# Performance work log

Measured on AMD Instinct MI355X. Metric: run time of the kernel, lower is better.

## Reference

```python
import jax, jax.numpy as jnp
import numpy as np

TEMPERATURE = 0.8
NEG_FILL = -1e-09  # faithful to original masked_fill value


def setup_inputs() -> dict:
    key = jax.random.key(0)
    k1, k2, k3, k4 = jax.random.split(key, 4)
    B, H, S, D = 2, 16, 2048, 128
    return {
        "key": jax.random.normal(k1, (B, H, S, D), dtype=jnp.float32),
        "value": jax.random.normal(k2, (B, H, S, D), dtype=jnp.float32),
        "query": jax.random.normal(k3, (B, H, S, D), dtype=jnp.float32),
        "mask": jax.random.randint(k4, (1, 1, S, S), 0, 2, dtype=jnp.int32),
    }


def reference(key, value, query, mask) -> jnp.ndarray:
    # scores: [B,H,S,S]
    scores = jnp.einsum("bhqd,bhkd->bhqk", query, key) / TEMPERATURE
    scores = jnp.where(mask == 0, jnp.asarray(NEG_FILL, scores.dtype), scores)
    probs = jax.nn.softmax(scores, axis=-1)
    # dropout p=0.0 -> identity
    return jnp.einsum("bhqk,bhkd->bhqd", probs, value)
```

## Files before the change

kernel.cpp:

```cpp
#include <hip/hip_runtime.h>
#include <hip/hip_bf16.h>
#include <stdint.h>

#define S_LEN 2048
#define HD 128
#define QBLK 128
#define KVBLK 64
#define TPB 512
#define NBH 32
#define NKT (S_LEN / KVBLK)
#define KIMG_TILE 16384

typedef __attribute__((ext_vector_type(8))) _Float16 f16x8;
typedef __attribute__((ext_vector_type(8))) short s16x8;
typedef __attribute__((ext_vector_type(4))) float f32x4;

__device__ __forceinline__ short f2h(float f) {
  _Float16 h = (_Float16)f;
  return __builtin_bit_cast(short, h);
}
__device__ __forceinline__ unsigned short f2b(float f) {
  union { float fv; unsigned u; } v; v.fv = f;
  unsigned r = v.u + 0x7fffu + ((v.u >> 16) & 1u);
  return (unsigned short)(r >> 16);
}
__device__ __forceinline__ float b2f(unsigned short h) {
  union { unsigned u; float fv; } v; v.u = ((unsigned)h) << 16; return v.fv;
}

typedef __attribute__((address_space(3))) uint32_t lds_u32_t;
typedef __attribute__((address_space(1))) const uint32_t glb_u32_t;
__device__ __forceinline__ void gll16(const void* g, void* l) {
  __builtin_amdgcn_global_load_lds((glb_u32_t*)g, (lds_u32_t*)l, 16, 0, 0);
}

__global__ __launch_bounds__(256) void prep_kv(
    const float* __restrict__ Kg, const float* __restrict__ Vg,
    char* __restrict__ KfI, char* __restrict__ VtI) {
  __shared__ __align__(16) char vlds[64 * 528];
  const int t = threadIdx.x;
  const int bh = blockIdx.x >> 5;
  const int kt = blockIdx.x & 31;
  const size_t base = ((size_t)bh * S_LEN + (size_t)kt * KVBLK) * HD;
  const size_t tbase = ((size_t)bh * NKT + kt) * KIMG_TILE;

  {
    const int row = t >> 2;
    const int c4 = (t & 3) * 32;
    const float* src = Kg + base + (size_t)row * HD + c4;
#pragma unroll
    for (int j8 = 0; j8 < 4; ++j8) {
      float4 a = *(const float4*)(src + j8 * 8);
      float4 b = *(const float4*)(src + j8 * 8 + 4);
      float vs[8] = {a.x, a.y, a.z, a.w, b.x, b.y, b.z, b.w};
      s16x8 h;
#pragma unroll
      for (int j = 0; j < 8; ++j) h[j] = f2h(vs[j]);
      int off = (row * 256 + (c4 + j8 * 8) * 2) ^ ((row & 7) << 4);
      *(s16x8*)(KfI + tbase + off) = h;
    }
  }

#pragma unroll
  for (int it = 0; it < 8; ++it) {
    int idx = it * 256 + t;
    int row = idx >> 5;
    int cb = (idx & 31) * 16;
    float4 v = *(const float4*)((const char*)(Vg + base + (size_t)row * HD) + cb);
    *(float4*)(vlds + row * 528 + cb) = v;
  }
  __syncthreads();
  {
    const int d = t & 127;
    const int kvb = (t >> 7) * 32;
#pragma unroll
    for (int jj = 0; jj < 4; ++jj) {
      s16x8 o;
#pragma unroll
      for (int j = 0; j < 8; ++j) {
        int kv = kvb + jj * 8 + j;
        float f = *(const float*)(vlds + kv * 528 + d * 4);
        o[j] = f2h(f);
      }
      int off = (d * 128 + (kvb + jj * 8) * 2) ^ ((d & 7) << 4);
      *(s16x8*)(VtI + tbase + off) = o;
    }
  }
}

#define BUFB 32768
#define SMEMF4 (2 * BUFB + 8 * 2048)

__global__ __launch_bounds__(TPB, 2) void attn_fwd4(
    const char* __restrict__ KfI, const char* __restrict__ VtI,
    const float* __restrict__ Qg, const int* __restrict__ Mg,
    float* __restrict__ Og) {
  __shared__ __align__(16) char smem[SMEMF4];
  char* Psm = smem + 2 * BUFB;

  const int tid = threadIdx.x;
  const int wave = tid >> 6;
  const int lane = tid & 63;
  const int lm = lane & 15;
  const int lg = lane >> 4;

  const int bh = blockIdx.x;
  const int q0 = blockIdx.y * QBLK;
  const int qrow0 = q0 + wave * 16;
  const size_t base = (size_t)bh * S_LEN * HD;
  const float* Qb = Qg + base;

  f16x8 qf[4];
#pragma unroll
  for (int c = 0; c < 4; ++c) {
    const float* src = Qb + (size_t)(qrow0 + lm) * HD + c * 32 + lg * 8;
    float4 a = *(const float4*)src;
    float4 b = *(const float4*)(src + 4);
    float qs[8] = {a.x, a.y, a.z, a.w, b.x, b.y, b.z, b.w};
    f16x8 f;
#pragma unroll
    for (int j = 0; j < 8; ++j) f[j] = (_Float16)(qs[j] * 1.25f);
    qf[c] = f;
  }

  f32x4 acc[8];
#pragma unroll
  for (int i = 0; i < 8; ++i) acc[i] = (f32x4){0.f, 0.f, 0.f, 0.f};
  float mrun[4] = {-1e30f, -1e30f, -1e30f, -1e30f};
  float lrun[4] = {0.f, 0.f, 0.f, 0.f};

  char* Pw = Psm + wave * 2048;
  const int wo = wave * 2048 + lane * 16;

  {
    const size_t tb = (size_t)bh * NKT * KIMG_TILE;
    char* B = smem;
    gll16(KfI + tb + wo,         B + wave * 2048);
    gll16(KfI + tb + wo + 1024,  B + wave * 2048 + 1024);
    gll16(VtI + tb + wo,         B + 16384 + wave * 2048);
    gll16(VtI + tb + wo + 1024,  B + 16384 + wave * 2048 + 1024);
  }
  int mk[4][4], mkn[4][4];
#pragma unroll
  for (int r = 0; r < 4; ++r) {
    const int* mr = Mg + (size_t)(qrow0 + lg * 4 + r) * S_LEN + lm;
#pragma unroll
    for (int st = 0; st < 4; ++st) mk[r][st] = mr[st * 16];
  }

  for (int kt = 0; kt < NKT; ++kt) {
    const int cur = kt & 1;
    char* Bc = smem + cur * BUFB;

    if (kt + 1 < NKT) {
      const size_t tb = ((size_t)bh * NKT + (kt + 1)) * KIMG_TILE;
      char* Bn = smem + (cur ^ 1) * BUFB;
      gll16(KfI + tb + wo,         Bn + wave * 2048);
      gll16(KfI + tb + wo + 1024,  Bn + wave * 2048 + 1024);
      gll16(VtI + tb + wo,         Bn + 16384 + wave * 2048);
      gll16(VtI + tb + wo + 1024,  Bn + 16384 + wave * 2048 + 1024);
      const int kv1 = (kt + 1) * KVBLK;
#pragma unroll
      for (int r = 0; r < 4; ++r) {
        const int* mr = Mg + (size_t)(qrow0 + lg * 4 + r) * S_LEN + kv1 + lm;
#pragma unroll
        for (int st = 0; st < 4; ++st) mkn[r][st] = mr[st * 16];
      }
      asm volatile("s_waitcnt vmcnt(20)" ::: "memory");
    } else {
      asm volatile("s_waitcnt vmcnt(0)" ::: "memory");
    }
    __builtin_amdgcn_sched_barrier(0);
    __builtin_amdgcn_s_barrier();

    __builtin_amdgcn_s_setprio(1);
    f32x4 sf[4];
#pragma unroll
    for (int st = 0; st < 4; ++st) {
      f32x4 c = (f32x4){0.f, 0.f, 0.f, 0.f};
#pragma unroll
      for (int ch = 0; ch < 4; ++ch) {
        int krow = st * 16 + lm;
        int byo = (krow * 256 + ch * 64 + lg * 16) ^ ((krow & 7) << 4);
        f16x8 kf = *(const f16x8*)(Bc + byo);
        c = __builtin_amdgcn_mfma_f32_16x16x32_f16(qf[ch], kf, c, 0, 0, 0);
      }
      sf[st] = c;
    }
    __builtin_amdgcn_s_setprio(0);

    float sc[4][4];
    float mx4[4];
#pragma unroll
    for (int r = 0; r < 4; ++r) {
      float mx = -1e30f;
#pragma unroll
      for (int st = 0; st < 4; ++st) {
        float s = sf[st][r];
        s = mk[r][st] ? s : -1e-9f;
        sc[r][st] = s;
        mx = fmaxf(mx, s);
      }
      mx = fmaxf(mx, __shfl_xor(mx, 1));
      mx = fmaxf(mx, __shfl_xor(mx, 2));
      mx = fmaxf(mx, __shfl_xor(mx, 4));
      mx = fmaxf(mx, __shfl_xor(mx, 8));
      mx4[r] = mx;
    }
    bool need = false;
#pragma unroll
    for (int r = 0; r < 4; ++r) need = need || (mx4[r] > mrun[r] + 8.f);
    if (__any(need)) {
#pragma unroll
      for (int r = 0; r < 4; ++r) {
        float mnew = fmaxf(mrun[r], mx4[r]);
        float scale = __expf(mrun[r] - mnew);
        lrun[r] *= scale;
        mrun[r] = mnew;
#pragma unroll
        for (int dt = 0; dt < 8; ++dt) acc[dt][r] *= scale;
      }
    }
    float pv[4][4];
#pragma unroll
    for (int r = 0; r < 4; ++r) {
      float ps = 0.f;
#pragma unroll
      for (int st = 0; st < 4; ++st) {
        float p = __expf(sc[r][st] - mrun[r]);
        pv[st][r] = p;
        ps += p;
      }
      ps += __shfl_xor(ps, 1);
      ps += __shfl_xor(ps, 2);
      ps += __shfl_xor(ps, 4);
      ps += __shfl_xor(ps, 8);
      lrun[r] += ps;
    }

#pragma unroll
    for (int st = 0; st < 4; ++st) {
#pragma unroll
      for (int r = 0; r < 4; ++r) {
        int row = lg * 4 + r;
        int byo = (row * 128 + (st * 16 + lm) * 2) ^ ((row & 7) << 4);
        *(short*)(Pw + byo) = f2h(pv[st][r]);
      }
    }
    asm volatile("s_waitcnt lgkmcnt(0)" ::: "memory");
    __builtin_amdgcn_sched_barrier(0);

    __builtin_amdgcn_s_setprio(1);
#pragma unroll
    for (int kk = 0; kk < 2; ++kk) {
      f16x8 pa = *(const f16x8*)(Pw + ((lm * 128 + kk * 64 + lg * 16) ^ ((lm & 7) << 4)));
#pragma unroll
      for (int dt = 0; dt < 8; ++dt) {
        int vrow = dt * 16 + lm;
        f16x8 vb = *(const f16x8*)(Bc + 16384 + ((vrow * 128 + kk * 64 + lg * 16) ^ ((lm & 7) << 4)));
        acc[dt] = __builtin_amdgcn_mfma_f32_16x16x32_f16(pa, vb, acc[dt], 0, 0, 0);
      }
    }
    __builtin_amdgcn_s_setprio(0);

    __builtin_amdgcn_sched_barrier(0);
    __builtin_amdgcn_s_barrier();

    if (kt + 1 < NKT) {
#pragma unroll
      for (int r = 0; r < 4; ++r)
#pragma unroll
        for (int st = 0; st < 4; ++st) mk[r][st] = mkn[r][st];
    }
  }

  float invl[4];
#pragma unroll
  for (int r = 0; r < 4; ++r) invl[r] = 1.f / lrun[r];
  float* ob = Og + base;
#pragma unroll
  for (int dt = 0; dt < 8; ++dt) {
#pragma unroll
    for (int r = 0; r < 4; ++r) {
      ob[(size_t)(qrow0 + lg * 4 + r) * HD + dt * 16 + lm] = acc[dt][r] * invl[r];
    }
  }
}

typedef __attribute__((ext_vector_type(8))) short bf16x8;
#define KSM_BYTES (KVBLK * HD * 2)
#define VSM_BYTES (HD * 72 * 2)
#define PSM_PER_WAVE (16 * 72 * 2)
#define SMEM_BYTES (2 * KSM_BYTES + VSM_BYTES + 8 * PSM_PER_WAVE)

__global__ __launch_bounds__(TPB, 2) void attn_fwd(
    const float* __restrict__ Kg, const float* __restrict__ Vg,
    const float* __restrict__ Qg, const int* __restrict__ Mg,
    float* __restrict__ Og) {
  __shared__ __align__(16) char smem[SMEM_BYTES];
  char* KsmH = smem;
  char* KsmL = smem + KSM_BYTES;
  char* Vsm = smem + 2 * KSM_BYTES;
  char* Psm = smem + 2 * KSM_BYTES + VSM_BYTES;

  const int tid = threadIdx.x;
  const int wave = tid >> 6;
  const int lane = tid & 63;
  const int lm = lane & 15;
  const int lg = lane >> 4;

  const int bh = blockIdx.x;
  const int q0 = blockIdx.y * QBLK;
  const int qrow0 = q0 + wave * 16;

  const size_t base = (size_t)bh * S_LEN * HD;
  const float* Kb = Kg + base;
  const float* Vb = Vg + base;
  const float* Qb = Qg + base;

  bf16x8 qhi[4], qlo[4];
#pragma unroll
  for (int c = 0; c < 4; ++c) {
    const float* src = Qb + (size_t)(qrow0 + lm) * HD + c * 32 + lg * 8;
    float4 a = *(const float4*)src;
    float4 b = *(const float4*)(src + 4);
    float qs[8] = {a.x, a.y, a.z, a.w, b.x, b.y, b.z, b.w};
    bf16x8 fh, fl;
#pragma unroll
    for (int j = 0; j < 8; ++j) {
      float v = qs[j] * 1.25f;
      unsigned short h = f2b(v);
      fh[j] = (short)h;
      fl[j] = (short)f2b(v - b2f(h));
    }
    qhi[c] = fh;
    qlo[c] = fl;
  }

  f32x4 acc[8];
#pragma unroll
  for (int i = 0; i < 8; ++i) acc[i] = (f32x4){0.f, 0.f, 0.f, 0.f};
  float mrun[4] = {-1e30f, -1e30f, -1e30f, -1e30f};
  float lrun[4] = {0.f, 0.f, 0.f, 0.f};

  char* Pw = Psm + wave * PSM_PER_WAVE;

  for (int kt = 0; kt < S_LEN / KVBLK; ++kt) {
    const int kv0 = kt * KVBLK;
    int mk[4][4];
#pragma unroll
    for (int r = 0; r < 4; ++r) {
      const int* mr = Mg + (size_t)(qrow0 + lg * 4 + r) * S_LEN + kv0 + lm;
#pragma unroll
      for (int st = 0; st < 4; ++st) mk[r][st] = mr[st * 16];
    }
    __syncthreads();
#pragma unroll
    for (int it = 0; it < 4; ++it) {
      int row = it * 16 + (tid >> 5);
      int col = (tid & 31) * 4;
      float4 v = *(const float4*)(Kb + (size_t)(kv0 + row) * HD + col);
      ushort4 hi, lo;
      hi.x = f2b(v.x); lo.x = f2b(v.x - b2f(hi.x));
      hi.y = f2b(v.y); lo.y = f2b(v.y - b2f(hi.y));
      hi.z = f2b(v.z); lo.z = f2b(v.z - b2f(hi.z));
      hi.w = f2b(v.w); lo.w = f2b(v.w - b2f(hi.w));
      int byo = (row * 256 + col * 2) ^ ((row & 7) << 4);
      *(ushort4*)(KsmH + byo) = hi;
      *(ushort4*)(KsmL + byo) = lo;
    }
    {
      int d = tid & 127;
      int kvh = (tid >> 7) * 16;
      const float* vc = Vb + (size_t)kv0 * HD + d;
#pragma unroll
      for (int j = 0; j < 4; ++j) {
        int kvb = kvh + j * 4;
        ushort4 h = make_ushort4(f2b(vc[(size_t)(kvb + 0) * HD]),
                                 f2b(vc[(size_t)(kvb + 1) * HD]),
                                 f2b(vc[(size_t)(kvb + 2) * HD]),
                                 f2b(vc[(size_t)(kvb + 3) * HD]));
        *(ushort4*)(Vsm + d * 144 + kvb * 2) = h;
      }
    }
    __syncthreads();

    f32x4 sf[4];
#pragma unroll
    for (int st = 0; st < 4; ++st) {
      f32x4 c = (f32x4){0.f, 0.f, 0.f, 0.f};
#pragma unroll
      for (int ch = 0; ch < 4; ++ch) {
        int krow = st * 16 + lm;
        int byo = (krow * 256 + (ch * 32 + lg * 8) * 2) ^ ((krow & 7) << 4);
        bf16x8 khi = *(const bf16x8*)(KsmH + byo);
        bf16x8 klo = *(const bf16x8*)(KsmL + byo);
        c = __builtin_amdgcn_mfma_f32_16x16x32_bf16(qhi[ch], khi, c, 0, 0, 0);
        c = __builtin_amdgcn_mfma_f32_16x16x32_bf16(qlo[ch], khi, c, 0, 0, 0);
        c = __builtin_amdgcn_mfma_f32_16x16x32_bf16(qhi[ch], klo, c, 0, 0, 0);
      }
      sf[st] = c;
    }

    float pv[4][4];
#pragma unroll
    for (int r = 0; r < 4; ++r) {
      float sc[4];
      float mx = -1e30f;
#pragma unroll
      for (int st = 0; st < 4; ++st) {
        float s = sf[st][r];
        sc[st] = mk[r][st] ? s : -1e-9f;
        mx = fmaxf(mx, sc[st]);
      }
      mx = fmaxf(mx, __shfl_xor(mx, 1));
      mx = fmaxf(mx, __shfl_xor(mx, 2));
      mx = fmaxf(mx, __shfl_xor(mx, 4));
      mx = fmaxf(mx, __shfl_xor(mx, 8));
      float mnew = fmaxf(mrun[r], mx);
      float scale = __expf(mrun[r] - mnew);
      float ps = 0.f;
#pragma unroll
      for (int st = 0; st < 4; ++st) {
        float p = __expf(sc[st] - mnew);
        pv[st][r] = p;
        ps += p;
      }
      ps += __shfl_xor(ps, 1);
      ps += __shfl_xor(ps, 2);
      ps += __shfl_xor(ps, 4);
      ps += __shfl_xor(ps, 8);
      lrun[r] = lrun[r] * scale + ps;
      mrun[r] = mnew;
#pragma unroll
      for (int dt = 0; dt < 8; ++dt) acc[dt][r] *= scale;
    }

#pragma unroll
    for (int st = 0; st < 4; ++st) {
#pragma unroll
      for (int r = 0; r < 4; ++r) {
        int row = lg * 4 + r;
        int col = st * 16 + lm;
        *(unsigned short*)(Pw + row * 144 + col * 2) = f2b(pv[st][r]);
      }
    }
    asm volatile("s_waitcnt lgkmcnt(0)" ::: "memory");
    __builtin_amdgcn_sched_barrier(0);

#pragma unroll
    for (int kk = 0; kk < 2; ++kk) {
      bf16x8 pa = *(const bf16x8*)(Pw + lm * 144 + kk * 64 + lg * 16);
#pragma unroll
      for (int dt = 0; dt < 8; ++dt) {
        bf16x8 vb = *(const bf16x8*)(Vsm + (dt * 16 + lm) * 144 + kk * 64 + lg * 16);
        acc[dt] = __builtin_amdgcn_mfma_f32_16x16x32_bf16(pa, vb, acc[dt], 0, 0, 0);
      }
    }
  }

  float invl[4];
#pragma unroll
  for (int r = 0; r < 4; ++r) invl[r] = 1.f / lrun[r];
  float* ob = Og + base;
#pragma unroll
  for (int dt = 0; dt < 8; ++dt) {
#pragma unroll
    for (int r = 0; r < 4; ++r) {
      ob[(size_t)(qrow0 + lg * 4 + r) * HD + dt * 16 + lm] = acc[dt][r] * invl[r];
    }
  }
}

extern "C" void kernel_launch(void* const* d_in, const int* in_sizes, int n_in,
                              void* d_out, int out_size, void* d_ws, size_t ws_size,
                              hipStream_t stream) {
  const float* key   = (const float*)d_in[0];
  const float* value = (const float*)d_in[1];
  const float* query = (const float*)d_in[2];
  const int*   mask  = (const int*)d_in[3];
  float* out = (float*)d_out;

  const size_t PLANE = (size_t)NBH * NKT * KIMG_TILE;
  if (ws_size >= 2 * PLANE) {
    char* kf = (char*)d_ws;
    char* vt = kf + PLANE;
    prep_kv<<<dim3(NBH * NKT), dim3(256), 0, stream>>>(key, value, kf, vt);
    attn_fwd4<<<dim3(NBH, S_LEN / QBLK), dim3(TPB), 0, stream>>>(kf, vt, query, mask, out);
  } else {
    attn_fwd<<<dim3(NBH, S_LEN / QBLK), dim3(TPB), 0, stream>>>(key, value, query, mask, out);
  }
}
```

Before: 337.6 us.

## Transpose MFMA operands to keep P in registers and drop LDS round-trip

The QK^T MFMA now takes K as the A operand, so each lane holds one query row's scores. That lets the row max and sum reduce with two shuffles instead of four per row, and packs P to fp16 in registers, moved via cross-lane shuffles instead of staging through LDS. The mask is read as int4 vectors and the output is stored as float4. The double-buffered K/V prefetch is removed in favour of single-buffer loads between two __syncthreads, which cuts LDS use but exposes global load latency each tile.

Result: slower. 360.1 us (+6.7%).

```diff
diff --git a/kernel.cpp b/kernel.cpp
--- a/kernel.cpp
+++ b/kernel.cpp
@@ -26,6 +26,9 @@
 }
 __device__ __forceinline__ float b2f(unsigned short h) {
   union { unsigned u; float fv; } v; v.u = ((unsigned)h) << 16; return v.fv;
+}
+__device__ __forceinline__ unsigned pkrtz(float a, float b) {
+  return __builtin_bit_cast(unsigned, __builtin_amdgcn_cvt_pkrtz(a, b));
 }
 
 typedef __attribute__((address_space(3))) uint32_t lds_u32_t;
@@ -88,15 +91,13 @@
   }
 }
 
-#define BUFB 32768
-#define SMEMF4 (2 * BUFB + 8 * 2048)
-
-__global__ __launch_bounds__(TPB, 2) void attn_fwd4(
+#define SMEMF5 32768
+
+__global__ __launch_bounds__(TPB, 2) void attn_fwd5(
     const char* __restrict__ KfI, const char* __restrict__ VtI,
     const float* __restrict__ Qg, const int* __restrict__ Mg,
     float* __restrict__ Og) {
-  __shared__ __align__(16) char smem[SMEMF4];
-  char* Psm = smem + 2 * BUFB;
+  __shared__ __align__(16) char smem[SMEMF5];
 
   const int tid = threadIdx.x;
   const int wave = tid >> 6;
@@ -126,52 +127,30 @@
   f32x4 acc[8];
 #pragma unroll
   for (int i = 0; i < 8; ++i) acc[i] = (f32x4){0.f, 0.f, 0.f, 0.f};
-  float mrun[4] = {-1e30f, -1e30f, -1e30f, -1e30f};
-  float lrun[4] = {0.f, 0.f, 0.f, 0.f};
-
-  char* Pw = Psm + wave * 2048;
+  float mrun = -1e30f;
+  float lrun = 0.f;
+
   const int wo = wave * 2048 + lane * 16;
-
-  {
-    const size_t tb = (size_t)bh * NKT * KIMG_TILE;
-    char* B = smem;
-    gll16(KfI + tb + wo,         B + wave * 2048);
-    gll16(KfI + tb + wo + 1024,  B + wave * 2048 + 1024);
-    gll16(VtI + tb + wo,         B + 16384 + wave * 2048);
-    gll16(VtI + tb + wo + 1024,  B + 16384 + wave * 2048 + 1024);
-  }
-  int mk[4][4], mkn[4][4];
-#pragma unroll
-  for (int r = 0; r < 4; ++r) {
-    const int* mr = Mg + (size_t)(qrow0 + lg * 4 + r) * S_LEN + lm;
-#pragma unroll
-    for (int st = 0; st < 4; ++st) mk[r][st] = mr[st * 16];
-  }
+  const int* Mrow = Mg + (size_t)(qrow0 + lm) * S_LEN + 4 * lg;
 
   for (int kt = 0; kt < NKT; ++kt) {
-    const int cur = kt & 1;
-    char* Bc = smem + cur * BUFB;
-
-    if (kt + 1 < NKT) {
-      const size_t tb = ((size_t)bh * NKT + (kt + 1)) * KIMG_TILE;
-      char* Bn = smem + (cur ^ 1) * BUFB;
-      gll16(KfI + tb + wo,         Bn + wave * 2048);
-      gll16(KfI + tb + wo + 1024,  Bn + wave * 2048 + 1024);
-      gll16(VtI + tb + wo,         Bn + 16384 + wave * 2048);
-      gll16(VtI + tb + wo + 1024,  Bn + 16384 + wave * 2048 + 1024);
-      const int kv1 = (kt + 1) * KVBLK;
-#pragma unroll
-      for (int r = 0; r < 4; ++r) {
-        const int* mr = Mg + (size_t)(qrow0 + lg * 4 + r) * S_LEN + kv1 + lm;
-#pragma unroll
-        for (int st = 0; st < 4; ++st) mkn[r][st] = mr[st * 16];
-      }
-      asm volatile("s_waitcnt vmcnt(20)" ::: "memory");
-    } else {
-      asm volatile("s_waitcnt vmcnt(0)" ::: "memory");
-    }
-    __builtin_amdgcn_sched_barrier(0);
-    __builtin_amdgcn_s_barrier();
+    const int kv0 = kt * KVBLK;
+
+    __syncthreads();
+
+    {
+      const size_t tb = ((size_t)bh * NKT + kt) * KIMG_TILE;
+      gll16(KfI + tb + wo,        smem + wave * 2048);
+      gll16(KfI + tb + wo + 1024, smem + wave * 2048 + 1024);
+      gll16(VtI + tb + wo,        smem + 16384 + wave * 2048);
+      gll16(VtI + tb + wo + 1024, smem + 16384 + wave * 2048 + 1024);
+    }
+    int4 mk4[4];
+#pragma unroll
+    for (int st = 0; st < 4; ++st)
+      mk4[st] = *(const int4*)(Mrow + kv0 + st * 16);
+
+    __syncthreads();
 
     __builtin_amdgcn_s_setprio(1);
     f32x4 sf[4];
@@ -182,108 +161,93 @@
       for (int ch = 0; ch < 4; ++ch) {
         int krow = st * 16 + lm;
         int byo = (krow * 256 + ch * 64 + lg * 16) ^ ((krow & 7) << 4);
-        f16x8 kf = *(const f16x8*)(Bc + byo);
-        c = __builtin_amdgcn_mfma_f32_16x16x32_f16(qf[ch], kf, c, 0, 0, 0);
+        f16x8 kf = *(const f16x8*)(smem + byo);
+        c = __builtin_amdgcn_mfma_f32_16x16x32_f16(kf, qf[ch], c, 0, 0, 0);
       }
       sf[st] = c;
     }
     __builtin_amdgcn_s_setprio(0);
 
-    float sc[4][4];
-    float mx4[4];
-#pragma unroll
-    for (int r = 0; r < 4; ++r) {
-      float mx = -1e30f;
-#pragma unroll
-      for (int st = 0; st < 4; ++st) {
-        float s = sf[st][r];
-        s = mk[r][st] ? s : -1e-9f;
-        sc[r][st] = s;
+    float p[4][4];
+    float mx = -1e30f;
+#pragma unroll
+    for (int st = 0; st < 4; ++st) {
+      int mr[4] = {mk4[st].x, mk4[st].y, mk4[st].z, mk4[st].w};
+#pragma unroll
+      for (int r = 0; r < 4; ++r) {
+        float s = mr[r] ? sf[st][r] : -1e-9f;
+        p[st][r] = s;
         mx = fmaxf(mx, s);
       }
-      mx = fmaxf(mx, __shfl_xor(mx, 1));
-      mx = fmaxf(mx, __shfl_xor(mx, 2));
-      mx = fmaxf(mx, __shfl_xor(mx, 4));
-      mx = fmaxf(mx, __shfl_xor(mx, 8));
-      mx4[r] = mx;
-    }
-    bool need = false;
-#pragma unroll
-    for (int r = 0; r < 4; ++r) need = need || (mx4[r] > mrun[r] + 8.f);
+    }
+    mx = fmaxf(mx, __shfl_xor(mx, 16));
+    mx = fmaxf(mx, __shfl_xor(mx, 32));
+
+    bool need = mx > mrun + 8.f;
     if (__any(need)) {
+      float mnew = fmaxf(mrun, mx);
+      float scale = __expf(mrun - mnew);
+      lrun *= scale;
+      mrun = mnew;
+#pragma unroll
+      for (int dt = 0; dt < 8; ++dt) acc[dt] *= scale;
+    }
+    float ps = 0.f;
+#pragma unroll
+    for (int st = 0; st < 4; ++st)
 #pragma unroll
       for (int r = 0; r < 4; ++r) {
-        float mnew = fmaxf(mrun[r], mx4[r]);
-        float scale = __expf(mrun[r] - mnew);
-        lrun[r] *= scale;
-        mrun[r] = mnew;
-#pragma unroll
-        for (int dt = 0; dt < 8; ++dt) acc[dt][r] *= scale;
-      }
-    }
-    float pv[4][4];
-#pragma unroll
-    for (int r = 0; r < 4; ++r) {
-      float ps = 0.f;
-#pragma unroll
-      for (int st = 0; st < 4; ++st) {
-        float p = __expf(sc[r][st] - mrun[r]);
-        pv[st][r] = p;
-        ps += p;
-      }
-      ps += __shfl_xor(ps, 1);
-      ps += __shfl_xor(ps, 2);
-      ps += __shfl_xor(ps, 4);
-      ps += __shfl_xor(ps, 8);
-      lrun[r] += ps;
-    }
-
-#pragma unroll
-    for (int st = 0; st < 4; ++st) {
-#pragma unroll
-      for (int r = 0; r < 4; ++r) {
-        int row = lg * 4 + r;
-        int byo = (row * 128 + (st * 16 + lm) * 2) ^ ((row & 7) << 4);
-        *(short*)(Pw + byo) = f2h(pv[st][r]);
-      }
-    }
-    asm volatile("s_waitcnt lgkmcnt(0)" ::: "memory");
-    __builtin_amdgcn_sched_barrier(0);
-
-    __builtin_amdgcn_s_setprio(1);
+        float e = __expf(p[st][r] - mrun);
+        p[st][r] = e;
+        ps += e;
+      }
+    ps += __shfl_xor(ps, 16);
+    ps += __shfl_xor(ps, 32);
+    lrun += ps;
+
+    unsigned w[4][2];
+#pragma unroll
+    for (int st = 0; st < 4; ++st)
+#pragma unroll
+      for (int rp = 0; rp < 2; ++rp)
+        w[st][rp] = pkrtz(p[st][2 * rp], p[st][2 * rp + 1]);
+
 #pragma unroll
     for (int kk = 0; kk < 2; ++kk) {
-      f16x8 pa = *(const f16x8*)(Pw + ((lm * 128 + kk * 64 + lg * 16) ^ ((lm & 7) << 4)));
+      int words[4];
+#pragma unroll
+      for (int i = 0; i < 4; ++i) {
+        int src = lm + 16 * ((lg & 1) * 2 + (i >> 1));
+        int wa = __shfl((int)w[2 * kk + 0][i & 1], src);
+        int wb = __shfl((int)w[2 * kk + 1][i & 1], src);
+        words[i] = (lg >> 1) ? wb : wa;
+      }
+      union { int v[4]; f16x8 h; } pb;
+      pb.v[0] = words[0]; pb.v[1] = words[1];
+      pb.v[2] = words[2]; pb.v[3] = words[3];
+
+      __builtin_amdgcn_s_setprio(1);
 #pragma unroll
       for (int dt = 0; dt < 8; ++dt) {
         int vrow = dt * 16 + lm;
-        f16x8 vb = *(const f16x8*)(Bc + 16384 + ((vrow * 128 + kk * 64 + lg * 16) ^ ((lm & 7) << 4)));
-        acc[dt] = __builtin_amdgcn_mfma_f32_16x16x32_f16(pa, vb, acc[dt], 0, 0, 0);
-      }
-    }
-    __builtin_amdgcn_s_setprio(0);
-
-    __builtin_amdgcn_sched_barrier(0);
-    __builtin_amdgcn_s_barrier();
-
-    if (kt + 1 < NKT) {
-#pragma unroll
-      for (int r = 0; r < 4; ++r)
-#pragma unroll
-        for (int st = 0; st < 4; ++st) mk[r][st] = mkn[r][st];
-    }
-  }
-
-  float invl[4];
-#pragma unroll
-  for (int r = 0; r < 4; ++r) invl[r] = 1.f / lrun[r];
-  float* ob = Og + base;
+        int byo = (vrow * 128 + (kk * 32 + lg * 8) * 2) ^ ((vrow & 7) << 4);
+        f16x8 va = *(const f16x8*)(smem + 16384 + byo);
+        acc[dt] = __builtin_amdgcn_mfma_f32_16x16x32_f16(va, pb.h, acc[dt], 0, 0, 0);
+      }
+      __builtin_amdgcn_s_setprio(0);
+    }
+  }
+
+  float invl = 1.f / lrun;
+  float* ob = Og + base + (size_t)(qrow0 + lm) * HD;
 #pragma unroll
   for (int dt = 0; dt < 8; ++dt) {
-#pragma unroll
-    for (int r = 0; r < 4; ++r) {
-      ob[(size_t)(qrow0 + lg * 4 + r) * HD + dt * 16 + lm] = acc[dt][r] * invl[r];
-    }
+    float4 o;
+    o.x = acc[dt][0] * invl;
+    o.y = acc[dt][1] * invl;
+    o.z = acc[dt][2] * invl;
+    o.w = acc[dt][3] * invl;
+    *(float4*)(ob + dt * 16 + 4 * lg) = o;
   }
 }
 
@@ -486,7 +450,7 @@
     char* kf = (char*)d_ws;
     char* vt = kf + PLANE;
     prep_kv<<<dim3(NBH * NKT), dim3(256), 0, stream>>>(key, value, kf, vt);
-    attn_fwd4<<<dim3(NBH, S_LEN / QBLK), dim3(TPB), 0, stream>>>(kf, vt, query, mask, out);
+    attn_fwd5<<<dim3(NBH, S_LEN / QBLK), dim3(TPB), 0, stream>>>(kf, vt, query, mask, out);
   } else {
     attn_fwd<<<dim3(NBH, S_LEN / QBLK), dim3(TPB), 0, stream>>>(key, value, query, mask, out);
   }
```
